# Kernel tuning notes

Hardware: AMD Instinct MI355X
Metric: run time of the kernel (lower is better)

The kernel has to match this reference:

```python
import jax, jax.numpy as jnp
import numpy as np

N, IN_DIM, OUT_DIM = 8192, 128, 64
NEG_INF = -9e15

def setup_inputs() -> dict:
    key = jax.random.key(0)
    k1, k2, k3, k4 = jax.random.split(key, 4)
    h = jax.random.normal(k1, (N, IN_DIM), dtype=jnp.float32)
    adj = jax.random.randint(k2, (N, N), 0, 2, dtype=jnp.int32)
    W = jax.random.normal(k3, (IN_DIM, OUT_DIM), dtype=jnp.float32) * (1.0 / np.sqrt(IN_DIM))
    a = jax.random.normal(k4, (2 * OUT_DIM,), dtype=jnp.float32)
    return {"h": h, "adj": adj, "W": W, "a": a}

def reference(h, adj, W, a):
    Wh = h @ W  # [N, F]
    F_ = Wh.shape[1]
    # additive decomposition of cat([Wh_i, Wh_j]) @ a == Wh_i@a1 + Wh_j@a2
    e_src = Wh @ a[:F_]   # [N]
    e_dst = Wh @ a[F_:]   # [N]
    e = jax.nn.leaky_relu(e_src[:, None] + e_dst[None, :], negative_slope=0.01)  # [N, N]
    attention = jnp.where(adj > 0, e, jnp.float32(NEG_INF))
    attention = jax.nn.softmax(attention, axis=1)
    h_prime = attention @ Wh  # [N, F]
    return jax.nn.elu(h_prime)
```

## Files before the change

### kernel.cpp

```cpp
#include <hip/hip_runtime.h>
#include <hip/hip_bf16.h>

typedef __attribute__((ext_vector_type(8))) short short8;
typedef __attribute__((ext_vector_type(4))) float f32x4;

#define NROW 8192
#define FDIM 64
#define INDIM 128
#define BK 64
#define LDP 72

__global__ __launch_bounds__(256) void k_wh(const float* __restrict__ h,
                                            const float* __restrict__ W,
                                            const float* __restrict__ a,
                                            __hip_bfloat16* __restrict__ WhT,
                                            float* __restrict__ s,
                                            float* __restrict__ d) {
  const int i = blockIdx.x * 4 + (threadIdx.x >> 6);
  const int f = threadIdx.x & 63;
  const float* hrow = h + (size_t)i * INDIM;
  float acc = 0.f;
#pragma unroll 8
  for (int k = 0; k < INDIM; ++k) acc = fmaf(hrow[k], W[k * FDIM + f], acc);
  WhT[(size_t)f * NROW + i] = __float2bfloat16(acc);
  float p1 = acc * a[f];
  float p2 = acc * a[FDIM + f];
#pragma unroll
  for (int m = 32; m; m >>= 1) {
    p1 += __shfl_xor(p1, m, 64);
    p2 += __shfl_xor(p2, m, 64);
  }
  if (f == 0) { s[i] = p1; d[i] = p2; }
}

__global__ __launch_bounds__(256) void k_dmax(const float* __restrict__ d,
                                              float* __restrict__ dmax) {
  __shared__ float red[256];
  float m = -3.4e38f;
  for (int j = threadIdx.x; j < NROW; j += 256) m = fmaxf(m, d[j]);
  red[threadIdx.x] = m;
  __syncthreads();
  for (int k = 128; k; k >>= 1) {
    if ((int)threadIdx.x < k) red[threadIdx.x] = fmaxf(red[threadIdx.x], red[threadIdx.x + k]);
    __syncthreads();
  }
  if (threadIdx.x == 0) *dmax = red[0];
}

__global__ __launch_bounds__(256) void k_main(const int* __restrict__ adj,
                                              const __hip_bfloat16* __restrict__ WhT,
                                              const float* __restrict__ sArr,
                                              const float* __restrict__ dArr,
                                              const float* __restrict__ dmaxPtr,
                                              float* __restrict__ accp,
                                              float* __restrict__ Zp,
                                              int splits) {
  __shared__ __hip_bfloat16 P[64 * LDP];
  __shared__ __hip_bfloat16 BT[64 * LDP];

  const int t = threadIdx.x;
  const int nchunk = (NROW / BK) / splits;
  const int tile = blockIdx.x / splits;
  const int split = blockIdx.x - tile * splits;
  const int row0 = tile * 64;
  const int j0 = split * nchunk * BK;
  const float dmax = *dmaxPtr;

  const int rb = t >> 5;
  const int jo = 2 * (t & 31);
  float sreg[8], mreg[8], zacc[8];
#pragma unroll
  for (int rr = 0; rr < 8; ++rr) {
    float sv = sArr[row0 + rb + 8 * rr];
    sreg[rr] = sv;
    float x = sv + dmax;
    mreg[rr] = (x >= 0.f) ? x : 0.01f * x;
    zacc[rr] = 0.f;
  }

  const int w = t >> 6, l = t & 63;
  const int rwave = 32 * (w & 1);
  const int nwave = 32 * (w >> 1);
  f32x4 acc00 = {0.f, 0.f, 0.f, 0.f}, acc01 = acc00, acc10 = acc00, acc11 = acc00;

  const int bfr = t >> 2, bj = (t & 3) * 16;

  int2 av[8];
  float2 dv;
  uint4 bv0, bv1;
  {
    const int jb = j0;
    dv = *(const float2*)(dArr + jb + jo);
#pragma unroll
    for (int rr = 0; rr < 8; ++rr)
      av[rr] = *(const int2*)(adj + (size_t)(row0 + rb + 8 * rr) * NROW + jb + jo);
    const uint4* bs = (const uint4*)(WhT + (size_t)bfr * NROW + jb + bj);
    bv0 = bs[0]; bv1 = bs[1];
  }

  for (int c = 0; c < nchunk; ++c) {
#pragma unroll
    for (int rr = 0; rr < 8; ++rr) {
      const int r = rb + 8 * rr;
      float x0 = sreg[rr] + dv.x; x0 = (x0 >= 0.f) ? x0 : 0.01f * x0;
      float x1 = sreg[rr] + dv.y; x1 = (x1 >= 0.f) ? x1 : 0.01f * x1;
      float w0 = (av[rr].x > 0) ? __expf(x0 - mreg[rr]) : 0.f;
      float w1 = (av[rr].y > 0) ? __expf(x1 - mreg[rr]) : 0.f;
      zacc[rr] += w0 + w1;
      __hip_bfloat162 pv;
      pv.x = __float2bfloat16(w0);
      pv.y = __float2bfloat16(w1);
      *(__hip_bfloat162*)&P[r * LDP + jo] = pv;
    }
    *(uint4*)&BT[bfr * LDP + bj] = bv0;
    *(uint4*)&BT[bfr * LDP + bj + 8] = bv1;
    __syncthreads();

    if (c + 1 < nchunk) {
      const int jb = j0 + (c + 1) * BK;
      dv = *(const float2*)(dArr + jb + jo);
#pragma unroll
      for (int rr = 0; rr < 8; ++rr)
        av[rr] = *(const int2*)(adj + (size_t)(row0 + rb + 8 * rr) * NROW + jb + jo);
      const uint4* bs = (const uint4*)(WhT + (size_t)bfr * NROW + jb + bj);
      bv0 = bs[0]; bv1 = bs[1];
    }

#pragma unroll
    for (int ks = 0; ks < 2; ++ks) {
      const int ko = ks * 32 + (l >> 4) * 8;
      short8 a0 = *(const short8*)&P[(rwave + (l & 15)) * LDP + ko];
      short8 a1 = *(const short8*)&P[(rwave + 16 + (l & 15)) * LDP + ko];
      short8 b0 = *(const short8*)&BT[(nwave + (l & 15)) * LDP + ko];
      short8 b1 = *(const short8*)&BT[(nwave + 16 + (l & 15)) * LDP + ko];
      acc00 = __builtin_amdgcn_mfma_f32_16x16x32_bf16(a0, b0, acc00, 0, 0, 0);
      acc01 = __builtin_amdgcn_mfma_f32_16x16x32_bf16(a0, b1, acc01, 0, 0, 0);
      acc10 = __builtin_amdgcn_mfma_f32_16x16x32_bf16(a1, b0, acc10, 0, 0, 0);
      acc11 = __builtin_amdgcn_mfma_f32_16x16x32_bf16(a1, b1, acc11, 0, 0, 0);
    }
    __syncthreads();
  }

#pragma unroll
  for (int rr = 0; rr < 8; ++rr) {
    float z = zacc[rr];
#pragma unroll
    for (int mk = 16; mk; mk >>= 1) z += __shfl_xor(z, mk, 64);
    if ((l & 31) == 0) Zp[(size_t)blockIdx.x * 64 + rb + 8 * rr] = z;
  }

  float* ab = accp + (size_t)blockIdx.x * 4096;
  {
    const int rbase = (l >> 4) * 4;
    const int cbase = l & 15;
#pragma unroll
    for (int rg = 0; rg < 4; ++rg) {
      ab[(rwave + rbase + rg) * 64 + (nwave + cbase)] = acc00[rg];
      ab[(rwave + rbase + rg) * 64 + (nwave + 16 + cbase)] = acc01[rg];
      ab[(rwave + 16 + rbase + rg) * 64 + (nwave + cbase)] = acc10[rg];
      ab[(rwave + 16 + rbase + rg) * 64 + (nwave + 16 + cbase)] = acc11[rg];
    }
  }
}

__global__ __launch_bounds__(256) void k_combine(const float* __restrict__ accp,
                                                 const float* __restrict__ Zp,
                                                 float* __restrict__ out,
                                                 int splits) {
  const int idx = blockIdx.x * 256 + threadIdx.x;
  const int r = idx >> 6, f = idx & 63;
  const int tile = r >> 6, rl = r & 63;
  float sum = 0.f, z = 0.f;
  for (int sp = 0; sp < splits; ++sp) {
    const int b = tile * splits + sp;
    sum += accp[(size_t)b * 4096 + rl * 64 + f];
    z += Zp[(size_t)b * 64 + rl];
  }
  const float v = sum / z;
  out[idx] = (v > 0.f) ? v : expm1f(v);
}

extern "C" void kernel_launch(void* const* d_in, const int* in_sizes, int n_in,
                              void* d_out, int out_size, void* d_ws, size_t ws_size,
                              hipStream_t stream) {
  const float* h = (const float*)d_in[0];
  const int* adj = (const int*)d_in[1];
  const float* W = (const float*)d_in[2];
  const float* a = (const float*)d_in[3];
  float* out = (float*)d_out;

  int splits = 8;
  auto need = [](int sp) -> size_t {
    return (size_t)1048576  + 65536  + 256  +
           (size_t)sp * 128 * 64 * 4  + (size_t)sp * 128 * 4096 * 4 ;
  };
  while (splits > 1 && need(splits) > ws_size) splits >>= 1;

  char* p = (char*)d_ws;
  __hip_bfloat16* WhT = (__hip_bfloat16*)p;
  float* s = (float*)(p + 1048576);
  float* d = (float*)(p + 1048576 + 32768);
  float* dmax = (float*)(p + 1048576 + 65536);
  float* Zp = (float*)(p + 1048576 + 65536 + 256);
  float* accp = (float*)((char*)Zp + (size_t)splits * 128 * 64 * 4);

  hipLaunchKernelGGL(k_wh, dim3(NROW / 4), dim3(256), 0, stream, h, W, a, WhT, s, d);
  hipLaunchKernelGGL(k_dmax, dim3(1), dim3(256), 0, stream, d, dmax);
  hipLaunchKernelGGL(k_main, dim3(128 * splits), dim3(256), 0, stream,
                     adj, WhT, s, d, dmax, accp, Zp, splits);
  hipLaunchKernelGGL(k_combine, dim3(out_size / 256), dim3(256), 0, stream,
                     accp, Zp, out, splits);
}
```

Measured before the change: 104.5 us.

## Build attention MFMA fragments directly in registers, dropping shared-memory staging

Each wave now owns 32 rows and computes the softmax weights for its MFMA A-fragment layout directly in registers. WhT B-fragments are loaded straight from global memory, so the shared-memory tiles and block barriers go away. The row panel grows to 128 and splits go from 8 to 16, so the grid size stays the same. The change also vectorizes the dmax reduction. The cost is that all four waves load the same WhT fragments redundantly from global or cache, and the partial buffers written and read by the combine step grow.

Result: slower. 112.5 us (+7.6%).

```diff
diff --git a/kernel.cpp b/kernel.cpp
--- a/kernel.cpp
+++ b/kernel.cpp
@@ -8,7 +8,15 @@
 #define FDIM 64
 #define INDIM 128
 #define BK 64
-#define LDP 72
+#define BM 128
+
+static __device__ __forceinline__ short bfb(float x) {
+  __hip_bfloat16 b = __float2bfloat16(x);
+  return *reinterpret_cast<short*>(&b);
+}
+static __device__ __forceinline__ float lrelu(float x) {
+  return (x >= 0.f) ? x : 0.01f * x;
+}
 
 __global__ __launch_bounds__(256) void k_wh(const float* __restrict__ h,
                                             const float* __restrict__ W,
@@ -37,7 +45,11 @@
                                               float* __restrict__ dmax) {
   __shared__ float red[256];
   float m = -3.4e38f;
-  for (int j = threadIdx.x; j < NROW; j += 256) m = fmaxf(m, d[j]);
+  const float4* dv4 = (const float4*)d;
+  for (int j = threadIdx.x; j < NROW / 4; j += 256) {
+    float4 v = dv4[j];
+    m = fmaxf(fmaxf(m, fmaxf(v.x, v.y)), fmaxf(v.z, v.w));
+  }
   red[threadIdx.x] = m;
   __syncthreads();
   for (int k = 128; k; k >>= 1) {
@@ -55,112 +67,120 @@
                                               float* __restrict__ accp,
                                               float* __restrict__ Zp,
                                               int splits) {
-  __shared__ __hip_bfloat16 P[64 * LDP];
-  __shared__ __hip_bfloat16 BT[64 * LDP];
-
   const int t = threadIdx.x;
-  const int nchunk = (NROW / BK) / splits;
-  const int tile = blockIdx.x / splits;
-  const int split = blockIdx.x - tile * splits;
-  const int row0 = tile * 64;
-  const int j0 = split * nchunk * BK;
+  const int w = t >> 6, l = t & 63;
+  const int lr = l & 15;
+  const int lk = l >> 4;
+  const int panel = blockIdx.x / splits;
+  const int split = blockIdx.x - panel * splits;
+  const int row0 = panel * BM + w * 32;
+  const int jspan = NROW / splits;
+  const int j0 = split * jspan;
+  const int nchunk = jspan / BK;
+
   const float dmax = *dmaxPtr;
-
-  const int rb = t >> 5;
-  const int jo = 2 * (t & 31);
-  float sreg[8], mreg[8], zacc[8];
-#pragma unroll
-  for (int rr = 0; rr < 8; ++rr) {
-    float sv = sArr[row0 + rb + 8 * rr];
-    sreg[rr] = sv;
-    float x = sv + dmax;
-    mreg[rr] = (x >= 0.f) ? x : 0.01f * x;
-    zacc[rr] = 0.f;
-  }
-
-  const int w = t >> 6, l = t & 63;
-  const int rwave = 32 * (w & 1);
-  const int nwave = 32 * (w >> 1);
-  f32x4 acc00 = {0.f, 0.f, 0.f, 0.f}, acc01 = acc00, acc10 = acc00, acc11 = acc00;
-
-  const int bfr = t >> 2, bj = (t & 3) * 16;
-
-  int2 av[8];
-  float2 dv;
-  uint4 bv0, bv1;
-  {
-    const int jb = j0;
-    dv = *(const float2*)(dArr + jb + jo);
-#pragma unroll
-    for (int rr = 0; rr < 8; ++rr)
-      av[rr] = *(const int2*)(adj + (size_t)(row0 + rb + 8 * rr) * NROW + jb + jo);
-    const uint4* bs = (const uint4*)(WhT + (size_t)bfr * NROW + jb + bj);
-    bv0 = bs[0]; bv1 = bs[1];
+  const float s0 = sArr[row0 + lr];
+  const float s1 = sArr[row0 + 16 + lr];
+  const float m0 = lrelu(s0 + dmax);
+  const float m1 = lrelu(s1 + dmax);
+
+  f32x4 acc[2][4];
+#pragma unroll
+  for (int ri = 0; ri < 2; ++ri)
+#pragma unroll
+    for (int nf = 0; nf < 4; ++nf) acc[ri][nf] = (f32x4){0.f, 0.f, 0.f, 0.f};
+  float z0 = 0.f, z1 = 0.f;
+
+  const int* adjr0 = adj + (size_t)(row0 + lr) * NROW + j0 + lk * 8;
+  const int* adjr1 = adjr0 + (size_t)16 * NROW;
+  const float* dp = dArr + j0 + lk * 8;
+  const __hip_bfloat16* bbase = WhT + (size_t)lr * NROW + j0 + lk * 8;
+
+  int4 av[2][2][2];
+#pragma unroll
+  for (int ks = 0; ks < 2; ++ks) {
+    av[0][ks][0] = *(const int4*)(adjr0 + ks * 32);
+    av[0][ks][1] = *(const int4*)(adjr0 + ks * 32 + 4);
+    av[1][ks][0] = *(const int4*)(adjr1 + ks * 32);
+    av[1][ks][1] = *(const int4*)(adjr1 + ks * 32 + 4);
   }
 
   for (int c = 0; c < nchunk; ++c) {
-#pragma unroll
-    for (int rr = 0; rr < 8; ++rr) {
-      const int r = rb + 8 * rr;
-      float x0 = sreg[rr] + dv.x; x0 = (x0 >= 0.f) ? x0 : 0.01f * x0;
-      float x1 = sreg[rr] + dv.y; x1 = (x1 >= 0.f) ? x1 : 0.01f * x1;
-      float w0 = (av[rr].x > 0) ? __expf(x0 - mreg[rr]) : 0.f;
-      float w1 = (av[rr].y > 0) ? __expf(x1 - mreg[rr]) : 0.f;
-      zacc[rr] += w0 + w1;
-      __hip_bfloat162 pv;
-      pv.x = __float2bfloat16(w0);
-      pv.y = __float2bfloat16(w1);
-      *(__hip_bfloat162*)&P[r * LDP + jo] = pv;
+    const int off = c * BK;
+    int4 cur[2][2][2];
+#pragma unroll
+    for (int ri = 0; ri < 2; ++ri)
+#pragma unroll
+      for (int ks = 0; ks < 2; ++ks) {
+        cur[ri][ks][0] = av[ri][ks][0];
+        cur[ri][ks][1] = av[ri][ks][1];
+      }
+    if (c + 1 < nchunk) {
+      const int noff = off + BK;
+#pragma unroll
+      for (int ks = 0; ks < 2; ++ks) {
+        av[0][ks][0] = *(const int4*)(adjr0 + noff + ks * 32);
+        av[0][ks][1] = *(const int4*)(adjr0 + noff + ks * 32 + 4);
+        av[1][ks][0] = *(const int4*)(adjr1 + noff + ks * 32);
+        av[1][ks][1] = *(const int4*)(adjr1 + noff + ks * 32 + 4);
+      }
     }
-    *(uint4*)&BT[bfr * LDP + bj] = bv0;
-    *(uint4*)&BT[bfr * LDP + bj + 8] = bv1;
-    __syncthreads();
-
-    if (c + 1 < nchunk) {
-      const int jb = j0 + (c + 1) * BK;
-      dv = *(const float2*)(dArr + jb + jo);
-#pragma unroll
-      for (int rr = 0; rr < 8; ++rr)
-        av[rr] = *(const int2*)(adj + (size_t)(row0 + rb + 8 * rr) * NROW + jb + jo);
-      const uint4* bs = (const uint4*)(WhT + (size_t)bfr * NROW + jb + bj);
-      bv0 = bs[0]; bv1 = bs[1];
+
+#pragma unroll
+    for (int ks = 0; ks < 2; ++ks) {
+      float4 dv0 = *(const float4*)(dp + off + ks * 32);
+      float4 dv1 = *(const float4*)(dp + off + ks * 32 + 4);
+      float dj[8] = {dv0.x, dv0.y, dv0.z, dv0.w, dv1.x, dv1.y, dv1.z, dv1.w};
+      const int* a0i = (const int*)&cur[0][ks][0];
+      const int* a1i = (const int*)&cur[1][ks][0];
+
+      short8 pa0, pa1;
+#pragma unroll
+      for (int q = 0; q < 8; ++q) {
+        float x0 = lrelu(s0 + dj[q]);
+        float x1 = lrelu(s1 + dj[q]);
+        float w0 = (a0i[q] > 0) ? __expf(x0 - m0) : 0.f;
+        float w1 = (a1i[q] > 0) ? __expf(x1 - m1) : 0.f;
+        z0 += w0;
+        z1 += w1;
+        pa0[q] = bfb(w0);
+        pa1[q] = bfb(w1);
+      }
+
+      const size_t boff = (size_t)(off + ks * 32);
+      short8 b0 = *(const short8*)(bbase + boff);
+      short8 b1 = *(const short8*)(bbase + boff + 16 * NROW);
+      short8 b2 = *(const short8*)(bbase + boff + 32 * NROW);
+      short8 b3 = *(const short8*)(bbase + boff + 48 * NROW);
+
+      acc[0][0] = __builtin_amdgcn_mfma_f32_16x16x32_bf16(pa0, b0, acc[0][0], 0, 0, 0);
+      acc[0][1] = __builtin_amdgcn_mfma_f32_16x16x32_bf16(pa0, b1, acc[0][1], 0, 0, 0);
+      acc[0][2] = __builtin_amdgcn_mfma_f32_16x16x32_bf16(pa0, b2, acc[0][2], 0, 0, 0);
+      acc[0][3] = __builtin_amdgcn_mfma_f32_16x16x32_bf16(pa0, b3, acc[0][3], 0, 0, 0);
+      acc[1][0] = __builtin_amdgcn_mfma_f32_16x16x32_bf16(pa1, b0, acc[1][0], 0, 0, 0);
+      acc[1][1] = __builtin_amdgcn_mfma_f32_16x16x32_bf16(pa1, b1, acc[1][1], 0, 0, 0);
+      acc[1][2] = __builtin_amdgcn_mfma_f32_16x16x32_bf16(pa1, b2, acc[1][2], 0, 0, 0);
+      acc[1][3] = __builtin_amdgcn_mfma_f32_16x16x32_bf16(pa1, b3, acc[1][3], 0, 0, 0);
     }
-
-#pragma unroll
-    for (int ks = 0; ks < 2; ++ks) {
-      const int ko = ks * 32 + (l >> 4) * 8;
-      short8 a0 = *(const short8*)&P[(rwave + (l & 15)) * LDP + ko];
-      short8 a1 = *(const short8*)&P[(rwave + 16 + (l & 15)) * LDP + ko];
-      short8 b0 = *(const short8*)&BT[(nwave + (l & 15)) * LDP + ko];
-      short8 b1 = *(const short8*)&BT[(nwave + 16 + (l & 15)) * LDP + ko];
-      acc00 = __builtin_amdgcn_mfma_f32_16x16x32_bf16(a0, b0, acc00, 0, 0, 0);
-      acc01 = __builtin_amdgcn_mfma_f32_16x16x32_bf16(a0, b1, acc01, 0, 0, 0);
-      acc10 = __builtin_amdgcn_mfma_f32_16x16x32_bf16(a1, b0, acc10, 0, 0, 0);
-      acc11 = __builtin_amdgcn_mfma_f32_16x16x32_bf16(a1, b1, acc11, 0, 0, 0);
-    }
-    __syncthreads();
-  }
-
-#pragma unroll
-  for (int rr = 0; rr < 8; ++rr) {
-    float z = zacc[rr];
-#pragma unroll
-    for (int mk = 16; mk; mk >>= 1) z += __shfl_xor(z, mk, 64);
-    if ((l & 31) == 0) Zp[(size_t)blockIdx.x * 64 + rb + 8 * rr] = z;
-  }
-
-  float* ab = accp + (size_t)blockIdx.x * 4096;
-  {
-    const int rbase = (l >> 4) * 4;
-    const int cbase = l & 15;
-#pragma unroll
-    for (int rg = 0; rg < 4; ++rg) {
-      ab[(rwave + rbase + rg) * 64 + (nwave + cbase)] = acc00[rg];
-      ab[(rwave + rbase + rg) * 64 + (nwave + 16 + cbase)] = acc01[rg];
-      ab[(rwave + 16 + rbase + rg) * 64 + (nwave + cbase)] = acc10[rg];
-      ab[(rwave + 16 + rbase + rg) * 64 + (nwave + 16 + cbase)] = acc11[rg];
-    }
-  }
+  }
+
+  z0 += __shfl_xor(z0, 16, 64);
+  z0 += __shfl_xor(z0, 32, 64);
+  z1 += __shfl_xor(z1, 16, 64);
+  z1 += __shfl_xor(z1, 32, 64);
+  if (l < 16) {
+    Zp[(size_t)blockIdx.x * BM + w * 32 + lr] = z0;
+    Zp[(size_t)blockIdx.x * BM + w * 32 + 16 + lr] = z1;
+  }
+
+  float* ab = accp + (size_t)blockIdx.x * (BM * 64);
+#pragma unroll
+  for (int ri = 0; ri < 2; ++ri)
+#pragma unroll
+    for (int nf = 0; nf < 4; ++nf)
+#pragma unroll
+      for (int q = 0; q < 4; ++q)
+        ab[(w * 32 + ri * 16 + lk * 4 + q) * 64 + nf * 16 + lr] = acc[ri][nf][q];
 }
 
 __global__ __launch_bounds__(256) void k_combine(const float* __restrict__ accp,
@@ -169,12 +189,12 @@
                                                  int splits) {
   const int idx = blockIdx.x * 256 + threadIdx.x;
   const int r = idx >> 6, f = idx & 63;
-  const int tile = r >> 6, rl = r & 63;
+  const int panel = r >> 7, rl = r & 127;
   float sum = 0.f, z = 0.f;
   for (int sp = 0; sp < splits; ++sp) {
-    const int b = tile * splits + sp;
-    sum += accp[(size_t)b * 4096 + rl * 64 + f];
-    z += Zp[(size_t)b * 64 + rl];
+    const int b = panel * splits + sp;
+    sum += accp[(size_t)b * (BM * 64) + rl * 64 + f];
+    z += Zp[(size_t)b * BM + rl];
   }
   const float v = sum / z;
   out[idx] = (v > 0.f) ? v : expm1f(v);
@@ -189,10 +209,12 @@
   const float* a = (const float*)d_in[3];
   float* out = (float*)d_out;
 
-  int splits = 8;
-  auto need = [](int sp) -> size_t {
+  const int npanel = NROW / BM;
+  int splits = 16;
+  auto need = [&](int sp) -> size_t {
     return (size_t)1048576  + 65536  + 256  +
-           (size_t)sp * 128 * 64 * 4  + (size_t)sp * 128 * 4096 * 4 ;
+           (size_t)sp * npanel * BM * 4  +
+           (size_t)sp * npanel * (BM * 64) * 4 ;
   };
   while (splits > 1 && need(splits) > ws_size) splits >>= 1;
 
@@ -202,11 +224,11 @@
   float* d = (float*)(p + 1048576 + 32768);
   float* dmax = (float*)(p + 1048576 + 65536);
   float* Zp = (float*)(p + 1048576 + 65536 + 256);
-  float* accp = (float*)((char*)Zp + (size_t)splits * 128 * 64 * 4);
+  float* accp = (float*)((char*)Zp + (size_t)splits * npanel * BM * 4);
 
   hipLaunchKernelGGL(k_wh, dim3(NROW / 4), dim3(256), 0, stream, h, W, a, WhT, s, d);
   hipLaunchKernelGGL(k_dmax, dim3(1), dim3(256), 0, stream, d, dmax);
-  hipLaunchKernelGGL(k_main, dim3(128 * splits), dim3(256), 0, stream,
+  hipLaunchKernelGGL(k_main, dim3(npanel * splits), dim3(256), 0, stream,
                      adj, WhT, s, d, dmax, accp, Zp, splits);
   hipLaunchKernelGGL(k_combine, dim3(out_size / 256), dim3(256), 0, stream,
                      accp, Zp, out, splits);
```
